# Kernel tuning notes

Measured on AMD Instinct MI355X. Metric: run time of the kernel, lower is better.

## Reference

```python
import jax, jax.numpy as jnp
import numpy as np

B, S, H = 8, 128, 768  # batch, seq_len, hidden (guide==vis)
EPS = 1e-12


def setup_inputs() -> dict:
    key = jax.random.key(0)
    ks = jax.random.split(key, 5)
    return {
        "seq_hiddens_x": jax.random.normal(ks[0], (B, S, H), jnp.float32),
        "seq_hiddens_y": jax.random.normal(ks[1], (B, S, H), jnp.float32),
        "cat_W": jax.random.normal(ks[2], (H, 2 * H), jnp.float32) * 0.02,
        "cat_b": jnp.zeros((H,), jnp.float32),
        "beta": jnp.zeros((H,), jnp.float32),
        "gamma": jnp.ones((H,), jnp.float32),
        "beta_W": jax.random.normal(ks[3], (H, H), jnp.float32) * 0.02,
        "gamma_W": jax.random.normal(ks[4], (H, H), jnp.float32) * 0.02,
    }


def reference(seq_hiddens_x, seq_hiddens_y, cat_W, cat_b, beta, gamma, beta_W, gamma_W):
    s = seq_hiddens_x.shape[1]
    # upper_reg2seq: flatten upper-triangular (i<=j) pairs, row-major
    ii, jj = np.triu_indices(s)
    guide = seq_hiddens_x[:, ii, :]    # (B, P, H)
    visible = seq_hiddens_y[:, jj, :]  # (B, P, H)

    # 'cat' branch: relu(Linear([guide; visible]))
    cat_pre = jax.nn.relu(
        jnp.einsum('bph,oh->bpo', jnp.concatenate([guide, visible], axis=-1), cat_W) + cat_b
    )

    # 'cln' branch: conditional LayerNorm(visible, cond=guide)
    # NOTE: original code uses std = (var + eps)**2 (not sqrt) -- replicated faithfully.
    b = jnp.einsum('bph,oh->bpo', guide, beta_W) + beta
    g = jnp.einsum('bph,oh->bpo', guide, gamma_W) + gamma
    mean = jnp.mean(visible, axis=-1, keepdims=True)
    cen = visible - mean
    var = jnp.mean(cen * cen, axis=-1, keepdims=True)
    std = (var + EPS) ** 2
    cln_pre = cen / std * g + b

    return (cat_pre + cln_pre) / 2.0
```

## Files before the change

kernel.cpp:

```cpp
#include <hip/hip_runtime.h>
#include <hip/hip_bf16.h>
#include <math.h>
#include <stdint.h>

#define S_LEN 128
#define H_DIM 768
#define B_DIM 8
#define NPAIR 8256
#define MROWS 1024
#define NTOT  3072
#define EPSC  1e-12f
#define CHUNK 8

typedef __bf16 bf16x8 __attribute__((ext_vector_type(8)));
typedef float  f32x4  __attribute__((ext_vector_type(4)));

static __device__ __forceinline__ unsigned short f2bf(float f) {
  union { float f; unsigned u; } a; a.f = f;
  unsigned u = a.u;
  u += 0x7fffu + ((u >> 16) & 1u);
  return (unsigned short)(u >> 16);
}
static __device__ __forceinline__ float bf2f(unsigned short s) {
  union { unsigned u; float f; } a; a.u = ((unsigned)s) << 16;
  return a.f;
}
static __device__ __forceinline__ float4 ld_bf4(const unsigned short* p) {
  ushort4 u = *(const ushort4*)p;
  float4 f; f.x = bf2f(u.x); f.y = bf2f(u.y); f.z = bf2f(u.z); f.w = bf2f(u.w);
  return f;
}

__global__ __launch_bounds__(256) void prep(const float* __restrict__ x,
                                            const float* __restrict__ y,
                                            const float* __restrict__ catW,
                                            const float* __restrict__ betaW,
                                            const float* __restrict__ gammaW,
                                            unsigned short* __restrict__ Xb,
                                            unsigned short* __restrict__ Yb,
                                            unsigned short* __restrict__ Wb,
                                            float* __restrict__ mean,
                                            float* __restrict__ inv) {
  const int bid = blockIdx.x;
  const int tid = threadIdx.x;
  if (bid < MROWS) {
    const int row = bid;
    float s = 0.f, s2 = 0.f;
    if (tid < 192) {
      const int o = tid * 4;
      float4 vx = *(const float4*)(x + (size_t)row * H_DIM + o);
      float4 vy = *(const float4*)(y + (size_t)row * H_DIM + o);
      ushort4 ox; ox.x = f2bf(vx.x); ox.y = f2bf(vx.y); ox.z = f2bf(vx.z); ox.w = f2bf(vx.w);
      ushort4 oy; oy.x = f2bf(vy.x); oy.y = f2bf(vy.y); oy.z = f2bf(vy.z); oy.w = f2bf(vy.w);
      *(ushort4*)(Xb + (size_t)row * H_DIM + o) = ox;
      *(ushort4*)(Yb + (size_t)row * H_DIM + o) = oy;
      s  = vy.x + vy.y + vy.z + vy.w;
      s2 = vy.x * vy.x + vy.y * vy.y + vy.z * vy.z + vy.w * vy.w;
    }
    for (int off = 32; off > 0; off >>= 1) { s += __shfl_down(s, off); s2 += __shfl_down(s2, off); }
    __shared__ float ls[4], ls2[4];
    if ((tid & 63) == 0) { ls[tid >> 6] = s; ls2[tid >> 6] = s2; }
    __syncthreads();
    if (tid == 0) {
      float S1 = ls[0] + ls[1] + ls[2] + ls[3];
      float S2 = ls2[0] + ls2[1] + ls2[2] + ls2[3];
      float m = S1 / H_DIM;
      float var = S2 / H_DIM - m * m;
      float st = var + EPSC;
      mean[row] = m;
      inv[row] = 1.0f / (st * st);
    }
  } else {
    int idx = (bid - MROWS) * 256 + tid;
    int e = idx * 4;
    int n = e / H_DIM, k = e % H_DIM;
    const float* src;
    if      (n < 768)  src = catW   + (size_t)n * 1536 + k;
    else if (n < 1536) src = betaW  + (size_t)(n - 768) * 768 + k;
    else if (n < 2304) src = gammaW + (size_t)(n - 1536) * 768 + k;
    else               src = catW   + (size_t)(n - 2304) * 1536 + 768 + k;
    float4 v = *(const float4*)src;
    ushort4 o; o.x = f2bf(v.x); o.y = f2bf(v.y); o.z = f2bf(v.z); o.w = f2bf(v.w);
    *(ushort4*)(Wb + e) = o;
  }
}

__device__ __forceinline__ void gload_lds16(const void* g, void* l) {
  __builtin_amdgcn_global_load_lds(
      (const __attribute__((address_space(1))) unsigned int*)(uintptr_t)g,
      (__attribute__((address_space(3))) unsigned int*)(uintptr_t)l,
      16, 0, 0);
}

__global__ __launch_bounds__(256) void gemm_bt(const unsigned short* __restrict__ Xb,
                                               const unsigned short* __restrict__ Yb,
                                               const unsigned short* __restrict__ Wb,
                                               unsigned short* __restrict__ P) {
  __shared__ unsigned short As[64 * 32];
  __shared__ unsigned short Bs[64 * 32];
  const int m0 = blockIdx.x * 64;
  const int n0 = blockIdx.y * 64;
  const unsigned short* A = (n0 < 2304) ? Xb : Yb;
  const unsigned short* Arow = A + (size_t)m0 * H_DIM;
  const unsigned short* Brow = Wb + (size_t)n0 * H_DIM;

  const int tid  = threadIdx.x;
  const int lane = tid & 63;
  const int wave = tid >> 6;
  const int wm = (wave >> 1) * 32;
  const int wn = (wave & 1) * 32;
  const int quad = lane >> 4;
  const int r    = lane & 15;

  const int ar = tid >> 2;
  const int ac = (tid & 3) * 8;

  f32x4 acc[2][2] = {};

  for (int k0 = 0; k0 < H_DIM; k0 += 32) {
    gload_lds16(Arow + (size_t)ar * H_DIM + k0 + ac, &As[tid * 8]);
    gload_lds16(Brow + (size_t)ar * H_DIM + k0 + ac, &Bs[tid * 8]);
    __syncthreads();

    bf16x8 af[2], bfr[2];
#pragma unroll
    for (int mi = 0; mi < 2; ++mi)
      af[mi] = *(const bf16x8*)&As[(wm + mi * 16 + r) * 32 + quad * 8];
#pragma unroll
    for (int ni = 0; ni < 2; ++ni)
      bfr[ni] = *(const bf16x8*)&Bs[(wn + ni * 16 + r) * 32 + quad * 8];
#pragma unroll
    for (int mi = 0; mi < 2; ++mi)
#pragma unroll
      for (int ni = 0; ni < 2; ++ni)
        acc[mi][ni] = __builtin_amdgcn_mfma_f32_16x16x32_bf16(af[mi], bfr[ni], acc[mi][ni], 0, 0, 0);
    __syncthreads();
  }

#pragma unroll
  for (int mi = 0; mi < 2; ++mi) {
#pragma unroll
    for (int ni = 0; ni < 2; ++ni) {
      const int row = m0 + wm + mi * 16 + quad * 4;
      const int col = n0 + wn + ni * 16 + r;
#pragma unroll
      for (int reg = 0; reg < 4; ++reg)
        P[(size_t)(row + reg) * NTOT + col] = f2bf(acc[mi][ni][reg]);
    }
  }
}

__global__ __launch_bounds__(192) void epilogue(const unsigned short* __restrict__ P,
                                                const float* __restrict__ Yf,
                                                const float* __restrict__ mean,
                                                const float* __restrict__ inv,
                                                const float* __restrict__ cat_b,
                                                const float* __restrict__ beta,
                                                const float* __restrict__ gamma,
                                                float* __restrict__ out) {
  const int b  = blockIdx.y;
  const int p0 = blockIdx.x * CHUNK;
  const int o  = threadIdx.x * 4;

  int i = (int)((257.0 - sqrt(257.0 * 257.0 - 8.0 * (double)p0)) * 0.5);
  if (i < 0) i = 0;
  if (i > S_LEN - 1) i = S_LEN - 1;
  while ((i + 1) * (256 - i) / 2 <= p0) ++i;
  while (i * (257 - i) / 2 > p0) --i;

  float4 cb = *(const float4*)(cat_b + o);
  float4 be = *(const float4*)(beta + o);
  float4 ga = *(const float4*)(gamma + o);

  size_t ri = (size_t)(b * S_LEN + i) * NTOT;
  float4 ax = ld_bf4(P + ri + o);
  float4 bx = ld_bf4(P + ri + 768 + o);
  float4 gx = ld_bf4(P + ri + 1536 + o);

#pragma unroll
  for (int t = 0; t < CHUNK; ++t) {
    const int p = p0 + t;
    bool moved = false;
    while ((i + 1) * (256 - i) / 2 <= p) { ++i; moved = true; }
    if (moved) {
      ri = (size_t)(b * S_LEN + i) * NTOT;
      ax = ld_bf4(P + ri + o);
      bx = ld_bf4(P + ri + 768 + o);
      gx = ld_bf4(P + ri + 1536 + o);
    }
    const int j = i + (p - i * (257 - i) / 2);
    const int rowj = b * S_LEN + j;
    float4 ay = ld_bf4(P + (size_t)rowj * NTOT + 2304 + o);
    float4 yv = *(const float4*)(Yf + (size_t)rowj * H_DIM + o);
    const float m  = mean[rowj];
    const float iv = inv[rowj];
    float4 rr;
    rr.x = 0.5f * (fmaxf(ax.x + ay.x + cb.x, 0.f) + (yv.x - m) * iv * (gx.x + ga.x) + bx.x + be.x);
    rr.y = 0.5f * (fmaxf(ax.y + ay.y + cb.y, 0.f) + (yv.y - m) * iv * (gx.y + ga.y) + bx.y + be.y);
    rr.z = 0.5f * (fmaxf(ax.z + ay.z + cb.z, 0.f) + (yv.z - m) * iv * (gx.z + ga.z) + bx.z + be.z);
    rr.w = 0.5f * (fmaxf(ax.w + ay.w + cb.w, 0.f) + (yv.w - m) * iv * (gx.w + ga.w) + bx.w + be.w);
    *(float4*)(out + ((size_t)b * NPAIR + p) * H_DIM + o) = rr;
  }
}

extern "C" void kernel_launch(void* const* d_in, const int* in_sizes, int n_in,
                              void* d_out, int out_size, void* d_ws, size_t ws_size,
                              hipStream_t stream) {
  const float* x      = (const float*)d_in[0];
  const float* y      = (const float*)d_in[1];
  const float* catW   = (const float*)d_in[2];
  const float* catb   = (const float*)d_in[3];
  const float* beta   = (const float*)d_in[4];
  const float* gamma  = (const float*)d_in[5];
  const float* betaW  = (const float*)d_in[6];
  const float* gammaW = (const float*)d_in[7];

  char* ws = (char*)d_ws;
  unsigned short* Xb   = (unsigned short*)(ws);
  unsigned short* Yb   = (unsigned short*)(ws + 1572864);
  unsigned short* Wb   = (unsigned short*)(ws + 3145728);
  unsigned short* P    = (unsigned short*)(ws + 7864320);
  float*          mean = (float*)(ws + 14155776);
  float*          inv  = (float*)(ws + 14159872);
  float*          out  = (float*)d_out;

  prep<<<MROWS + 2304, 256, 0, stream>>>(x, y, catW, betaW, gammaW, Xb, Yb, Wb, mean, inv);
  gemm_bt<<<dim3(16, 48), 256, 0, stream>>>(Xb, Yb, Wb, P);
  epilogue<<<dim3(NPAIR / CHUNK, B_DIM), 192, 0, stream>>>(P, y, mean, inv, catb, beta, gamma, out);
}
```

Baseline: 239.2 us.

## Rework pair epilogue: row-paired blocks, fp32 projections, precentered Y, nontemporal stores

The epilogue now gives each block a balanced pair of triangle rows (i and 127-i), split into two halves, with batch interleaved in the block index. This removes the per-chunk row search and reloads the guide projections only when the row changes. The GEMM writes fp32 projections instead of bf16, and prep precomputes the normalised visible rows (y-mean)*inv so the epilogue reads one array instead of y plus mean and inv. Output is written with nontemporal stores to avoid polluting the cache with the large result. The cost is a larger intermediate buffer and more GEMM store traffic, plus only 1024 blocks each running a long serial loop.

```diff
diff --git a/kernel.cpp b/kernel.cpp
--- a/kernel.cpp
+++ b/kernel.cpp
@@ -10,7 +10,6 @@
 #define MROWS 1024
 #define NTOT  3072
 #define EPSC  1e-12f
-#define CHUNK 8
 
 typedef __bf16 bf16x8 __attribute__((ext_vector_type(8)));
 typedef float  f32x4  __attribute__((ext_vector_type(4)));
@@ -20,15 +19,6 @@
   unsigned u = a.u;
   u += 0x7fffu + ((u >> 16) & 1u);
   return (unsigned short)(u >> 16);
-}
-static __device__ __forceinline__ float bf2f(unsigned short s) {
-  union { unsigned u; float f; } a; a.u = ((unsigned)s) << 16;
-  return a.f;
-}
-static __device__ __forceinline__ float4 ld_bf4(const unsigned short* p) {
-  ushort4 u = *(const ushort4*)p;
-  float4 f; f.x = bf2f(u.x); f.y = bf2f(u.y); f.z = bf2f(u.z); f.w = bf2f(u.w);
-  return f;
 }
 
 __global__ __launch_bounds__(256) void prep(const float* __restrict__ x,
@@ -39,17 +29,17 @@
                                             unsigned short* __restrict__ Xb,
                                             unsigned short* __restrict__ Yb,
                                             unsigned short* __restrict__ Wb,
-                                            float* __restrict__ mean,
-                                            float* __restrict__ inv) {
+                                            float* __restrict__ CY) {
   const int bid = blockIdx.x;
   const int tid = threadIdx.x;
   if (bid < MROWS) {
     const int row = bid;
     float s = 0.f, s2 = 0.f;
+    float4 vy = make_float4(0.f, 0.f, 0.f, 0.f);
     if (tid < 192) {
       const int o = tid * 4;
       float4 vx = *(const float4*)(x + (size_t)row * H_DIM + o);
-      float4 vy = *(const float4*)(y + (size_t)row * H_DIM + o);
+      vy = *(const float4*)(y + (size_t)row * H_DIM + o);
       ushort4 ox; ox.x = f2bf(vx.x); ox.y = f2bf(vx.y); ox.z = f2bf(vx.z); ox.w = f2bf(vx.w);
       ushort4 oy; oy.x = f2bf(vy.x); oy.y = f2bf(vy.y); oy.z = f2bf(vy.z); oy.w = f2bf(vy.w);
       *(ushort4*)(Xb + (size_t)row * H_DIM + o) = ox;
@@ -58,7 +48,7 @@
       s2 = vy.x * vy.x + vy.y * vy.y + vy.z * vy.z + vy.w * vy.w;
     }
     for (int off = 32; off > 0; off >>= 1) { s += __shfl_down(s, off); s2 += __shfl_down(s2, off); }
-    __shared__ float ls[4], ls2[4];
+    __shared__ float ls[4], ls2[4], smv[2];
     if ((tid & 63) == 0) { ls[tid >> 6] = s; ls2[tid >> 6] = s2; }
     __syncthreads();
     if (tid == 0) {
@@ -67,8 +57,17 @@
       float m = S1 / H_DIM;
       float var = S2 / H_DIM - m * m;
       float st = var + EPSC;
-      mean[row] = m;
-      inv[row] = 1.0f / (st * st);
+      smv[0] = m;
+      smv[1] = 1.0f / (st * st);
+    }
+    __syncthreads();
+    if (tid < 192) {
+      const int o = tid * 4;
+      const float m = smv[0], iv = smv[1];
+      float4 cy;
+      cy.x = (vy.x - m) * iv; cy.y = (vy.y - m) * iv;
+      cy.z = (vy.z - m) * iv; cy.w = (vy.w - m) * iv;
+      *(float4*)(CY + (size_t)row * H_DIM + o) = cy;
     }
   } else {
     int idx = (bid - MROWS) * 256 + tid;
@@ -95,7 +94,7 @@
 __global__ __launch_bounds__(256) void gemm_bt(const unsigned short* __restrict__ Xb,
                                                const unsigned short* __restrict__ Yb,
                                                const unsigned short* __restrict__ Wb,
-                                               unsigned short* __restrict__ P) {
+                                               float* __restrict__ P) {
   __shared__ unsigned short As[64 * 32];
   __shared__ unsigned short Bs[64 * 32];
   const int m0 = blockIdx.x * 64;
@@ -145,61 +144,54 @@
       const int col = n0 + wn + ni * 16 + r;
 #pragma unroll
       for (int reg = 0; reg < 4; ++reg)
-        P[(size_t)(row + reg) * NTOT + col] = f2bf(acc[mi][ni][reg]);
-    }
-  }
-}
-
-__global__ __launch_bounds__(192) void epilogue(const unsigned short* __restrict__ P,
-                                                const float* __restrict__ Yf,
-                                                const float* __restrict__ mean,
-                                                const float* __restrict__ inv,
+        P[(size_t)(row + reg) * NTOT + col] = acc[mi][ni][reg];
+    }
+  }
+}
+
+__global__ __launch_bounds__(192) void epilogue(const float* __restrict__ P,
+                                                const float* __restrict__ CY,
                                                 const float* __restrict__ cat_b,
                                                 const float* __restrict__ beta,
                                                 const float* __restrict__ gamma,
                                                 float* __restrict__ out) {
-  const int b  = blockIdx.y;
-  const int p0 = blockIdx.x * CHUNK;
+  const int b    = blockIdx.x & 7;
+  const int q    = blockIdx.x >> 3;
+  const int ii   = q >> 1;
+  const int half = q & 1;
+  const int i1 = ii, i2 = 127 - ii;
+  const int n1 = 128 - i1;
+  const int t0 = half ? 65 : 0;
+  const int t1 = half ? 129 : 65;
   const int o  = threadIdx.x * 4;
-
-  int i = (int)((257.0 - sqrt(257.0 * 257.0 - 8.0 * (double)p0)) * 0.5);
-  if (i < 0) i = 0;
-  if (i > S_LEN - 1) i = S_LEN - 1;
-  while ((i + 1) * (256 - i) / 2 <= p0) ++i;
-  while (i * (257 - i) / 2 > p0) --i;
 
   float4 cb = *(const float4*)(cat_b + o);
   float4 be = *(const float4*)(beta + o);
   float4 ga = *(const float4*)(gamma + o);
 
-  size_t ri = (size_t)(b * S_LEN + i) * NTOT;
-  float4 ax = ld_bf4(P + ri + o);
-  float4 bx = ld_bf4(P + ri + 768 + o);
-  float4 gx = ld_bf4(P + ri + 1536 + o);
-
-#pragma unroll
-  for (int t = 0; t < CHUNK; ++t) {
-    const int p = p0 + t;
-    bool moved = false;
-    while ((i + 1) * (256 - i) / 2 <= p) { ++i; moved = true; }
-    if (moved) {
-      ri = (size_t)(b * S_LEN + i) * NTOT;
-      ax = ld_bf4(P + ri + o);
-      bx = ld_bf4(P + ri + 768 + o);
-      gx = ld_bf4(P + ri + 1536 + o);
-    }
-    const int j = i + (p - i * (257 - i) / 2);
+  int icur = -1;
+  float4 ax, bx, gx;
+  ax = bx = gx = make_float4(0.f, 0.f, 0.f, 0.f);
+  for (int t = t0; t < t1; ++t) {
+    int i, j, p;
+    if (t < n1) { i = i1; j = i1 + t;       p = i1 * (257 - i1) / 2 + t; }
+    else        { int tt = t - n1; i = i2; j = i2 + tt; p = i2 * (257 - i2) / 2 + tt; }
+    if (i != icur) {
+      icur = i;
+      const float* ri = P + (size_t)(b * S_LEN + i) * NTOT;
+      ax = *(const float4*)(ri + o);
+      bx = *(const float4*)(ri + 768 + o);
+      gx = *(const float4*)(ri + 1536 + o);
+    }
     const int rowj = b * S_LEN + j;
-    float4 ay = ld_bf4(P + (size_t)rowj * NTOT + 2304 + o);
-    float4 yv = *(const float4*)(Yf + (size_t)rowj * H_DIM + o);
-    const float m  = mean[rowj];
-    const float iv = inv[rowj];
-    float4 rr;
-    rr.x = 0.5f * (fmaxf(ax.x + ay.x + cb.x, 0.f) + (yv.x - m) * iv * (gx.x + ga.x) + bx.x + be.x);
-    rr.y = 0.5f * (fmaxf(ax.y + ay.y + cb.y, 0.f) + (yv.y - m) * iv * (gx.y + ga.y) + bx.y + be.y);
-    rr.z = 0.5f * (fmaxf(ax.z + ay.z + cb.z, 0.f) + (yv.z - m) * iv * (gx.z + ga.z) + bx.z + be.z);
-    rr.w = 0.5f * (fmaxf(ax.w + ay.w + cb.w, 0.f) + (yv.w - m) * iv * (gx.w + ga.w) + bx.w + be.w);
-    *(float4*)(out + ((size_t)b * NPAIR + p) * H_DIM + o) = rr;
+    float4 ay = *(const float4*)(P + (size_t)rowj * NTOT + 2304 + o);
+    float4 cy = *(const float4*)(CY + (size_t)rowj * H_DIM + o);
+    f32x4 rr;
+    rr[0] = 0.5f * (fmaxf(ax.x + ay.x + cb.x, 0.f) + cy.x * (gx.x + ga.x) + bx.x + be.x);
+    rr[1] = 0.5f * (fmaxf(ax.y + ay.y + cb.y, 0.f) + cy.y * (gx.y + ga.y) + bx.y + be.y);
+    rr[2] = 0.5f * (fmaxf(ax.z + ay.z + cb.z, 0.f) + cy.z * (gx.z + ga.z) + bx.z + be.z);
+    rr[3] = 0.5f * (fmaxf(ax.w + ay.w + cb.w, 0.f) + cy.w * (gx.w + ga.w) + bx.w + be.w);
+    __builtin_nontemporal_store(rr, (f32x4*)(out + ((size_t)b * NPAIR + p) * H_DIM + o));
   }
 }
 
@@ -216,15 +208,14 @@
   const float* gammaW = (const float*)d_in[7];
 
   char* ws = (char*)d_ws;
-  unsigned short* Xb   = (unsigned short*)(ws);
-  unsigned short* Yb   = (unsigned short*)(ws + 1572864);
-  unsigned short* Wb   = (unsigned short*)(ws + 3145728);
-  unsigned short* P    = (unsigned short*)(ws + 7864320);
-  float*          mean = (float*)(ws + 14155776);
-  float*          inv  = (float*)(ws + 14159872);
-  float*          out  = (float*)d_out;
-
-  prep<<<MROWS + 2304, 256, 0, stream>>>(x, y, catW, betaW, gammaW, Xb, Yb, Wb, mean, inv);
+  unsigned short* Xb = (unsigned short*)(ws);
+  unsigned short* Yb = (unsigned short*)(ws + 1572864);
+  unsigned short* Wb = (unsigned short*)(ws + 3145728);
+  float*          P  = (float*)(ws + 7864320);
+  float*          CY = (float*)(ws + 20447232);
+  float*          out = (float*)d_out;
+
+  prep<<<MROWS + 2304, 256, 0, stream>>>(x, y, catW, betaW, gammaW, Xb, Yb, Wb, CY);
   gemm_bt<<<dim3(16, 48), 256, 0, stream>>>(Xb, Yb, Wb, P);
-  epilogue<<<dim3(NPAIR / CHUNK, B_DIM), 192, 0, stream>>>(P, y, mean, inv, catb, beta, gamma, out);
-}
+  epilogue<<<1024, 192, 0, stream>>>(P, CY, catb, beta, gamma, out);
+}
```

After: 251.9 us. +5.3%, slower.
